# Optimization experiments

Hardware: AMD Instinct MI355X
Metric: run time of the kernel (lower is better)

## Reference

```python
import jax, jax.numpy as jnp
import numpy as np

ENT_SIZE = 250000
REL_SIZE = 64
EMBED = 128
B = 32768
K = 8


def setup_inputs() -> dict:
    key = jax.random.key(0)
    ks = jax.random.split(key, 9)
    initrange = 0.5 / EMBED
    u = lambda k, n: jax.random.uniform(k, (n, EMBED), jnp.float32, -initrange, initrange)
    V = ENT_SIZE + REL_SIZE  # unified vocab: entities first, then relations
    return {
        "in_ent_w": u(ks[0], ENT_SIZE),
        "out_ent_w": u(ks[1], ENT_SIZE),
        "in_rel_w": u(ks[2], REL_SIZE),
        "out_rel_w": u(ks[3], REL_SIZE),
        "in_map_w": u(ks[4], REL_SIZE),
        "out_map_w": u(ks[5], REL_SIZE),
        "input_labels": jax.random.randint(ks[6], (B,), 0, V, jnp.int32),
        "pos_labels": jax.random.randint(ks[7], (B,), 0, V, jnp.int32),
        "neg_labels": jax.random.randint(ks[8], (B, K), 0, V, jnp.int32),
    }


def _map(ent, mapping):
    # project ent onto the hyperplane normal to normalize(mapping)  (TransH-style)
    n = mapping / jnp.maximum(jnp.linalg.norm(mapping, axis=-1, keepdims=True), 1e-12)
    return ent - jnp.sum(ent * n, axis=-1, keepdims=True) * n


def _pair_embs(iid, pid, is_ent_i, is_ent_p, in_ent_w, out_ent_w, in_rel_w, out_rel_w, in_map_w, out_map_w):
    """Per-row (input_emb, output_emb) per the 4 mask branches, plus the stable
    permutation that reproduces torch's boolean-mask + concat row ordering."""
    rel_size = in_rel_w.shape[0]
    iid_r = jnp.minimum(iid, rel_size - 1)  # clip: only used where label is a relation
    pid_r = jnp.minimum(pid, rel_size - 1)
    e_in = in_ent_w[iid]        # [N, D]
    r_in = in_rel_w[iid_r]
    e_out = out_ent_w[pid]
    r_out = out_rel_w[pid_r]
    mp_in = in_map_w[pid_r]
    mp_out = out_map_w[iid_r]
    mi = is_ent_i[:, None]
    mp = is_ent_p[:, None]
    inp = jnp.where(mi, jnp.where(mp, e_in, _map(e_in, mp_in)), r_in)
    out = jnp.where(mp, jnp.where(mi, e_out, _map(e_out, mp_out)), r_out)
    # branch key: 0=(ent,ent) 1=(ent,rel) 2=(rel,ent) 3=(rel,rel) -> concat order
    branch = (~is_ent_i).astype(jnp.int32) * 2 + (~is_ent_p).astype(jnp.int32)
    perm = jnp.argsort(branch, stable=True)
    return inp[perm], out[perm]


def reference(in_ent_w, out_ent_w, in_rel_w, out_rel_w, in_map_w, out_map_w,
              input_labels, pos_labels, neg_labels):
    ent_size = in_ent_w.shape[0]
    b, k = neg_labels.shape
    neg_flat = neg_labels.reshape(-1)

    # reverse_id_map: entity labels keep id, relation labels offset by ent_size
    to_id = lambda lab: jnp.where(lab < ent_size, lab, lab - ent_size)
    is_ent = lambda lab: lab < ent_size

    iid, pid, nid = to_id(input_labels), to_id(pos_labels), to_id(neg_flat)
    ii, ip, inn = is_ent(input_labels), is_ent(pos_labels), is_ent(neg_flat)

    Ws = (in_ent_w, out_ent_w, in_rel_w, out_rel_w, in_map_w, out_map_w)

    inp_pos, out_pos = _pair_embs(iid, pid, ii, ip, *Ws)
    iid_rep = jnp.repeat(iid, k)
    ii_rep = jnp.repeat(ii, k)
    inp_neg, out_neg = _pair_embs(iid_rep, nid, ii_rep, inn, *Ws)

    log_pos = jax.nn.log_sigmoid(jnp.sum(out_pos * inp_pos, axis=-1))          # [B]
    log_neg = jax.nn.log_sigmoid(jnp.sum(out_neg * (-inp_neg), axis=-1))       # [B*K]
    log_neg = log_neg.reshape(b, k).sum(axis=1)                                # [B]
    return -(log_pos + log_neg)
```

## Files before the change

kernel.cpp:

```cpp
#include <hip/hip_runtime.h>
#include <hip/hip_bf16.h>
#include <stdint.h>

#define ENT 250000
#define RELSZ 64
#define D 128
#define BATCH 32768
#define KNEG 8


__device__ __forceinline__ float logsig(float x) {
  return fminf(x, 0.f) - log1pf(expf(-fabsf(x)));
}

__global__ void k_prep(const float* __restrict__ in_rel, const float* __restrict__ out_rel,
                       const float* __restrict__ in_map, const float* __restrict__ out_map,
                       const int* __restrict__ in_lab, const int* __restrict__ pos_lab,
                       const int* __restrict__ neg_lab,
                       float* __restrict__ t1, float* __restrict__ t2, float* __restrict__ RR,
                       int* __restrict__ C, uint16_t* __restrict__ rank_pos,
                       uint16_t* __restrict__ rank_neg, float* __restrict__ out) {
  __shared__ float ls[4];
  __shared__ float sri[2][128];
  __shared__ int wc[4][4];
  int blk = blockIdx.x, t = threadIdx.x;

  if (blk >= 1152) {
    int sub = t >> 7, tt = t & 127;
    int p = (blk - 1152) * 2 + sub;
    float im = in_map[p * D + tt], om = out_map[p * D + tt];
    float ro = out_rel[p * D + tt], ri = in_rel[p * D + tt];
    float v, r, n_im, n_om;
    v = im * im;
#pragma unroll
    for (int off = 32; off > 0; off >>= 1) v += __shfl_xor(v, off, 64);
    if ((t & 63) == 0) ls[t >> 6] = v;
    __syncthreads();
    r = ls[sub * 2] + ls[sub * 2 + 1];
    n_im = im / fmaxf(sqrtf(r), 1e-12f);
    __syncthreads();
    v = om * om;
#pragma unroll
    for (int off = 32; off > 0; off >>= 1) v += __shfl_xor(v, off, 64);
    if ((t & 63) == 0) ls[t >> 6] = v;
    __syncthreads();
    r = ls[sub * 2] + ls[sub * 2 + 1];
    n_om = om / fmaxf(sqrtf(r), 1e-12f);
    __syncthreads();
    v = n_im * ro;
#pragma unroll
    for (int off = 32; off > 0; off >>= 1) v += __shfl_xor(v, off, 64);
    if ((t & 63) == 0) ls[t >> 6] = v;
    __syncthreads();
    float d1 = ls[sub * 2] + ls[sub * 2 + 1];
    __syncthreads();
    v = n_om * ri;
#pragma unroll
    for (int off = 32; off > 0; off >>= 1) v += __shfl_xor(v, off, 64);
    if ((t & 63) == 0) ls[t >> 6] = v;
    __syncthreads();
    float d2 = ls[sub * 2] + ls[sub * 2 + 1];
    t1[p * D + tt] = ro - d1 * n_im;
    t2[p * D + tt] = ri - d2 * n_om;
    sri[sub][tt] = ri;
    __syncthreads();
    int half = t >> 7, lq = t & 127;
    if (lq < RELSZ) {
      int pr = (blk - 1152) * 2 + half;
      const float* rq = out_rel + lq * D;
      const float* s = sri[half];
      float acc = 0.f;
#pragma unroll 8
      for (int d = 0; d < D; d += 4) {
        float4 r4 = *(const float4*)(rq + d);
        acc += s[d] * r4.x + s[d + 1] * r4.y + s[d + 2] * r4.z + s[d + 3] * r4.w;
      }
      RR[pr * RELSZ + lq] = acc;
    }
    return;
  }

  int wave = t >> 6, lane = t & 63;
  int key, i;
  bool is_pos = blk < 128;
  if (is_pos) {
    i = blk * 256 + t;
    int il = in_lab[i], pl = pos_lab[i];
    key = ((il >= ENT) ? 2 : 0) | ((pl >= ENT) ? 1 : 0);
  } else {
    i = (blk - 128) * 256 + t;
    int il = in_lab[i >> 3], nl = neg_lab[i];
    key = ((il >= ENT) ? 2 : 0) | ((nl >= ENT) ? 1 : 0);
  }
  unsigned long long m[4];
#pragma unroll
  for (int v = 0; v < 4; v++) m[v] = __ballot(key == v);
  if (lane < 4) wc[wave][lane] = __popcll(m[lane]);
  int wrank = __popcll(m[key] & ((1ull << lane) - 1ull));
  __syncthreads();
  if (t < 4) {
    int s = wc[0][t] + wc[1][t] + wc[2][t] + wc[3][t];
    int idx = is_pos ? (t * 128 + blk) : (512 + t * 1024 + (blk - 128));
    C[idx] = s;
  }
  int wpre = 0;
  for (int w = 0; w < wave; w++) wpre += wc[w][key];
  uint16_t rk = (uint16_t)(wpre + wrank);
  if (is_pos) { rank_pos[i] = rk; out[i] = 0.f; }
  else        { rank_neg[i] = rk; }
}

__global__ void k_scan(int* __restrict__ C) {
  int t = threadIdx.x, lane = t & 63, w = t >> 6;
  int base = t * 18;
  int v[18];
  int s = 0;
#pragma unroll
  for (int j = 0; j < 18; j++) { v[j] = C[base + j]; s += v[j]; }
  int inc = s;
#pragma unroll
  for (int off = 1; off < 64; off <<= 1) {
    int x = __shfl_up(inc, off, 64);
    if (lane >= off) inc += x;
  }
  __shared__ int wsum[4];
  if (lane == 63) wsum[w] = inc;
  __syncthreads();
  int wpre = 0;
  for (int i = 0; i < w; i++) wpre += wsum[i];
  int run = wpre + inc - s;
#pragma unroll
  for (int j = 0; j < 18; j++) { C[base + j] = run; run += v[j]; }
}

__global__ void k_main(const float* __restrict__ in_ent, const float* __restrict__ out_ent,
                       const float* __restrict__ t1, const float* __restrict__ t2,
                       const float* __restrict__ RR,
                       const int* __restrict__ in_lab, const int* __restrict__ pos_lab,
                       const int* __restrict__ neg_lab,
                       const int* __restrict__ C, const uint16_t* __restrict__ rank_pos,
                       const uint16_t* __restrict__ rank_neg, float* __restrict__ out) {
  int blk = blockIdx.x, t = threadIdx.x;
  int wave = t >> 6, lane = t & 63;
  int q = lane & 7, g = lane >> 3;

  bool is_pos = blk < 1024;
  int w = is_pos ? (blk * 4 + wave) : ((blk - 1024) * 4 + wave);
  int i = w * 8 + g;

  int il, o;
  if (is_pos) { il = in_lab[i]; o = pos_lab[i]; }
  else        { il = in_lab[w]; o = neg_lab[i]; }
  bool ei = il < ENT;
  int iid = ei ? il : il - ENT;
  bool eo = o < ENT;
  int oid = eo ? o : o - ENT;
  int key = (ei ? 0 : 2) | (eo ? 0 : 1);

  int rk = is_pos ? (int)rank_pos[i] : (int)rank_neg[i];
  int cidx = is_pos ? (key * 128 + (i >> 8)) : (512 + key * 1024 + (i >> 8));
  int cbase = C[cidx];

  const float* Lp = (ei ? in_ent + (size_t)iid * D : t2 + (size_t)iid * D) + q * 4;
  const float* Rp = (eo ? out_ent + (size_t)oid * D : t1 + (size_t)oid * D) + q * 4;
  float4 L0 = *(const float4*)(Lp);
  float4 L1 = *(const float4*)(Lp + 32);
  float4 L2 = *(const float4*)(Lp + 64);
  float4 L3 = *(const float4*)(Lp + 96);
  float4 R0 = *(const float4*)(Rp);
  float4 R1 = *(const float4*)(Rp + 32);
  float4 R2 = *(const float4*)(Rp + 64);
  float4 R3 = *(const float4*)(Rp + 96);

  float p = L0.x * R0.x + L0.y * R0.y + L0.z * R0.z + L0.w * R0.w +
            L1.x * R1.x + L1.y * R1.y + L1.z * R1.z + L1.w * R1.w +
            L2.x * R2.x + L2.y * R2.y + L2.z * R2.z + L2.w * R2.w +
            L3.x * R3.x + L3.y * R3.y + L3.z * R3.z + L3.w * R3.w;
#pragma unroll
  for (int off = 4; off > 0; off >>= 1) p += __shfl_xor(p, off, 64);

  if (q == 0) {
    float dot = p;
    if (!ei && !eo) dot = RR[iid * RELSZ + oid];
    int dest;
    float val;
    if (is_pos) { dest = cbase + rk;                 val = logsig(dot); }
    else        { dest = (cbase + rk - BATCH) >> 3;  val = logsig(-dot); }
    atomicAdd(out + dest, -val);
  }
}

extern "C" void kernel_launch(void* const* d_in, const int* in_sizes, int n_in,
                              void* d_out, int out_size, void* d_ws, size_t ws_size,
                              hipStream_t stream) {
  const float* in_ent  = (const float*)d_in[0];
  const float* out_ent = (const float*)d_in[1];
  const float* in_rel  = (const float*)d_in[2];
  const float* out_rel = (const float*)d_in[3];
  const float* in_map  = (const float*)d_in[4];
  const float* out_map = (const float*)d_in[5];
  const int* in_lab  = (const int*)d_in[6];
  const int* pos_lab = (const int*)d_in[7];
  const int* neg_lab = (const int*)d_in[8];

  char* ws = (char*)d_ws;
  float*    t1       = (float*)(ws + 0);
  float*    t2       = (float*)(ws + 32768);
  float*    RR       = (float*)(ws + 65536);
  int*      C        = (int*)(ws + 81920);
  uint16_t* rank_pos = (uint16_t*)(ws + 100352);
  uint16_t* rank_neg = (uint16_t*)(ws + 165888);
  float*    out      = (float*)d_out;

  k_prep<<<1184, 256, 0, stream>>>(in_rel, out_rel, in_map, out_map,
                                   in_lab, pos_lab, neg_lab,
                                   t1, t2, RR, C, rank_pos, rank_neg, out);
  k_scan<<<1, 256, 0, stream>>>(C);
  k_main<<<9216, 256, 0, stream>>>(in_ent, out_ent, t1, t2, RR,
                                   in_lab, pos_lab, neg_lab,
                                   C, rank_pos, rank_neg, out);
}
```

Before: 45.00 us.

## Remap main kernel to 4 lanes per row and merge negative atomics

Each row's dot product is now handled by 4 lanes instead of 8, with 8 float4 loads per lane. A wave covers 16 rows, so the grid is halved, and a launch-bounds hint is added. For the negative rows, the 8 partial log-sigmoid values that share one output slot are summed with shuffles, so a single atomic replaces eight when all of them agree on the destination. This aims to cut atomic traffic and raise memory-level parallelism per thread, at the cost of higher register use and extra shuffles.

```diff
diff --git a/kernel.cpp b/kernel.cpp
--- a/kernel.cpp
+++ b/kernel.cpp
@@ -133,24 +133,25 @@
   for (int j = 0; j < 18; j++) { C[base + j] = run; run += v[j]; }
 }
 
-__global__ void k_main(const float* __restrict__ in_ent, const float* __restrict__ out_ent,
-                       const float* __restrict__ t1, const float* __restrict__ t2,
-                       const float* __restrict__ RR,
-                       const int* __restrict__ in_lab, const int* __restrict__ pos_lab,
-                       const int* __restrict__ neg_lab,
-                       const int* __restrict__ C, const uint16_t* __restrict__ rank_pos,
-                       const uint16_t* __restrict__ rank_neg, float* __restrict__ out) {
+__global__ void __launch_bounds__(256, 4)
+k_main(const float* __restrict__ in_ent, const float* __restrict__ out_ent,
+       const float* __restrict__ t1, const float* __restrict__ t2,
+       const float* __restrict__ RR,
+       const int* __restrict__ in_lab, const int* __restrict__ pos_lab,
+       const int* __restrict__ neg_lab,
+       const int* __restrict__ C, const uint16_t* __restrict__ rank_pos,
+       const uint16_t* __restrict__ rank_neg, float* __restrict__ out) {
   int blk = blockIdx.x, t = threadIdx.x;
   int wave = t >> 6, lane = t & 63;
-  int q = lane & 7, g = lane >> 3;
-
-  bool is_pos = blk < 1024;
-  int w = is_pos ? (blk * 4 + wave) : ((blk - 1024) * 4 + wave);
-  int i = w * 8 + g;
+  int q = lane & 3, g = lane >> 2;
+
+  bool is_pos = blk < 512;
+  int w = (is_pos ? blk : blk - 512) * 4 + wave;
+  int i = w * 16 + g;
 
   int il, o;
   if (is_pos) { il = in_lab[i]; o = pos_lab[i]; }
-  else        { il = in_lab[w]; o = neg_lab[i]; }
+  else        { il = in_lab[i >> 3]; o = neg_lab[i]; }
   bool ei = il < ENT;
   int iid = ei ? il : il - ENT;
   bool eo = o < ENT;
@@ -163,30 +164,44 @@
 
   const float* Lp = (ei ? in_ent + (size_t)iid * D : t2 + (size_t)iid * D) + q * 4;
   const float* Rp = (eo ? out_ent + (size_t)oid * D : t1 + (size_t)oid * D) + q * 4;
-  float4 L0 = *(const float4*)(Lp);
-  float4 L1 = *(const float4*)(Lp + 32);
-  float4 L2 = *(const float4*)(Lp + 64);
-  float4 L3 = *(const float4*)(Lp + 96);
-  float4 R0 = *(const float4*)(Rp);
-  float4 R1 = *(const float4*)(Rp + 32);
-  float4 R2 = *(const float4*)(Rp + 64);
-  float4 R3 = *(const float4*)(Rp + 96);
-
-  float p = L0.x * R0.x + L0.y * R0.y + L0.z * R0.z + L0.w * R0.w +
-            L1.x * R1.x + L1.y * R1.y + L1.z * R1.z + L1.w * R1.w +
-            L2.x * R2.x + L2.y * R2.y + L2.z * R2.z + L2.w * R2.w +
-            L3.x * R3.x + L3.y * R3.y + L3.z * R3.z + L3.w * R3.w;
-#pragma unroll
-  for (int off = 4; off > 0; off >>= 1) p += __shfl_xor(p, off, 64);
-
-  if (q == 0) {
-    float dot = p;
-    if (!ei && !eo) dot = RR[iid * RELSZ + oid];
-    int dest;
-    float val;
-    if (is_pos) { dest = cbase + rk;                 val = logsig(dot); }
-    else        { dest = (cbase + rk - BATCH) >> 3;  val = logsig(-dot); }
-    atomicAdd(out + dest, -val);
+  float4 L[8], R[8];
+#pragma unroll
+  for (int k = 0; k < 8; k++) L[k] = *(const float4*)(Lp + k * 16);
+#pragma unroll
+  for (int k = 0; k < 8; k++) R[k] = *(const float4*)(Rp + k * 16);
+
+  float p = 0.f;
+#pragma unroll
+  for (int k = 0; k < 8; k++)
+    p += L[k].x * R[k].x + L[k].y * R[k].y + L[k].z * R[k].z + L[k].w * R[k].w;
+  p += __shfl_xor(p, 1, 64);
+  p += __shfl_xor(p, 2, 64);
+
+  float dot = p;
+  if (!ei && !eo) dot = RR[iid * RELSZ + oid];
+
+  if (is_pos) {
+    if (q == 0) atomicAdd(out + cbase + rk, -logsig(dot));
+    return;
+  }
+
+  int dest = (cbase + rk - BATCH) >> 3;
+  float myval = (q == 0) ? -logsig(-dot) : 0.f;
+  float v = myval;
+  int d = dest;
+  int eq = 1;
+#pragma unroll
+  for (int off = 4; off <= 16; off <<= 1) {
+    float vv = __shfl_xor(v, off, 64);
+    int dd = __shfl_xor(d, off, 64);
+    int ee = __shfl_xor(eq, off, 64);
+    eq = eq & ee & (dd == d ? 1 : 0);
+    v += vv;
+  }
+  if (eq) {
+    if (lane == 0 || lane == 32) atomicAdd(out + d, v);
+  } else if (q == 0) {
+    atomicAdd(out + dest, myval);
   }
 }
 
@@ -216,7 +231,7 @@
                                    in_lab, pos_lab, neg_lab,
                                    t1, t2, RR, C, rank_pos, rank_neg, out);
   k_scan<<<1, 256, 0, stream>>>(C);
-  k_main<<<9216, 256, 0, stream>>>(in_ent, out_ent, t1, t2, RR,
+  k_main<<<4608, 256, 0, stream>>>(in_ent, out_ent, t1, t2, RR,
                                    in_lab, pos_lab, neg_lab,
                                    C, rank_pos, rank_neg, out);
 }
```

Result: faster. 43.97 us (median of 2 runs) (-2.3%).
